# Performance work log

Hardware: AMD Instinct MI355X
Metric: run time of the kernel (lower is better)

Reference implementation:

```python
import jax, jax.numpy as jnp
import numpy as np
from jax import lax

TAU = 2.0
VTH = 1.0
EPS = 1e-5


def heaviside(x):
    return (x >= 0.0).astype(x.dtype)


def lif_scan(x):
    """x: [T, ...]; LIF with decay_input=True, v_reset=0 (hard reset)."""
    def step(v, xt):
        v = v + (xt - v) / TAU
        s = heaviside(v - VTH)
        v = v * (1.0 - s)
        return v, s
    _, out = lax.scan(step, jnp.zeros_like(x[0]), x)
    return out


def conv2d(x, w):
    return lax.conv_general_dilated(x, w, (1, 1), 'SAME',
                                    dimension_numbers=('NCHW', 'OIHW', 'NCHW'))


def bn(x, g, b, m, v):
    inv = lax.rsqrt(v + EPS)
    return (x - m[None, :, None, None]) * (g * inv)[None, :, None, None] + b[None, :, None, None]


def maxpool2(x):
    return lax.reduce_window(x, -jnp.inf, lax.max, (1, 1, 2, 2), (1, 1, 2, 2), 'VALID')


def conv_block(x, w, g, b, m, v, pool):
    T, B = x.shape[:2]
    y = x.reshape((T * B,) + x.shape[2:])
    y = bn(conv2d(y, w), g, b, m, v)
    y = y.reshape((T, B) + y.shape[1:])
    y = lif_scan(y)
    if pool:
        y = y.reshape((T * B,) + y.shape[2:])
        y = maxpool2(y)
        y = y.reshape((T, B) + y.shape[1:])
    return y


def setup_inputs() -> dict:
    key = jax.random.key(0)
    ks = jax.random.split(key, 12)
    x = jax.random.normal(ks[0], (8, 128, 3, 32, 32), jnp.float32)
    w1 = jax.random.normal(ks[1], (64, 3, 3, 3), jnp.float32) * 0.1
    w2 = jax.random.normal(ks[2], (128, 64, 3, 3), jnp.float32) * 0.05
    w3 = jax.random.normal(ks[3], (256, 128, 3, 3), jnp.float32) * 0.05
    fc1_w = jax.random.normal(ks[4], (512, 16384), jnp.float32) * 0.01
    raw = jax.random.normal(ks[5], (10, 512), jnp.float32)
    Q, _ = jnp.linalg.qr(raw.T)  # 10 <= 512: orthogonal prototypes
    protos = Q.T[:10]
    d = dict(x=x, w1=w1, w2=w2, w3=w3, fc1_w=fc1_w, protos=protos)
    for i, c in zip((1, 2, 3), (64, 128, 256)):
        d[f'g{i}'] = jnp.ones((c,), jnp.float32)
        d[f'b{i}'] = jnp.zeros((c,), jnp.float32)
        d[f'm{i}'] = jax.random.normal(jax.random.fold_in(key, 100 + i), (c,), jnp.float32) * 0.1
        d[f'var{i}'] = jax.random.uniform(jax.random.fold_in(key, 200 + i), (c,), jnp.float32) + 0.5
    return d


def reference(x, w1, g1, b1, m1, var1, w2, g2, b2, m2, var2,
              w3, g3, b3, m3, var3, fc1_w, protos):
    h = conv_block(x, w1, g1, b1, m1, var1, pool=False)   # [T,B,64,32,32]
    h = conv_block(h, w2, g2, b2, m2, var2, pool=True)    # [T,B,128,16,16]
    h = conv_block(h, w3, g3, b3, m3, var3, pool=True)    # [T,B,256,8,8]
    T, B = h.shape[:2]
    h = h.reshape(T, B, -1)                               # [T,B,16384]
    h = jnp.einsum('tbd,fd->tbf', h, fc1_w)
    h = lif_scan(h)                                        # [T,B,512]
    feat = h.mean(axis=0)                                  # [B,512]
    fn = feat / jnp.clip(jnp.linalg.norm(feat, axis=1, keepdims=True), 1e-12)
    pn = protos / jnp.clip(jnp.linalg.norm(protos, axis=1, keepdims=True), 1e-12)
    return fn @ pn.T * 10.0                                # [B,10]
```

## Files before the change

kernel.cpp:

```cpp
#include <hip/hip_runtime.h>
#include <stdint.h>

#define EPS 1e-5f

typedef __attribute__((ext_vector_type(4))) float f32x4;
typedef __attribute__((ext_vector_type(8))) __bf16 bf16x8;

__device__ __forceinline__ void gl_lds16(const void* g, void* l) {
    __builtin_amdgcn_global_load_lds(
        (const __attribute__((address_space(1))) void*)g,
        (__attribute__((address_space(3))) void*)l, 16, 0, 0);
}

__device__ __forceinline__ unsigned short f2bf(float f) {
    unsigned u = __builtin_bit_cast(unsigned, f);
    unsigned r = (u + 0x7FFFu + ((u >> 16) & 1u)) >> 16;
    return (unsigned short)r;
}
__device__ __forceinline__ float bf2f(unsigned short h) {
    unsigned u = ((unsigned)h) << 16;
    return __builtin_bit_cast(float, u);
}

__device__ __forceinline__ uint4 expand8(unsigned int bt) {
    uint4 val;
    val.x = ((bt & 1u) ? 0x3F80u : 0u)  | ((bt & 2u) ? 0x3F800000u : 0u);
    val.y = ((bt & 4u) ? 0x3F80u : 0u)  | ((bt & 8u) ? 0x3F800000u : 0u);
    val.z = ((bt & 16u) ? 0x3F80u : 0u) | ((bt & 32u) ? 0x3F800000u : 0u);
    val.w = ((bt & 64u) ? 0x3F80u : 0u) | ((bt & 128u) ? 0x3F800000u : 0u);
    return val;
}

#define OFF_W2S   0ULL
#define OFF_W3S   442368ULL
#define OFF_FCS   2211840ULL
#define OFF_S1M   52543488ULL
#define OFF_S2PM  60932096ULL
#define OFF_S3    65126400ULL
#define OFF_PRE4P 98680832ULL
#define OFF_FEAT  115458048ULL
#define OFF_PN    115720192ULL

__global__ void repack_w2s(const float* __restrict__ w2, unsigned short* __restrict__ out) {
    int i = blockIdx.x * 256 + threadIdx.x;
    if (i >= 73728) return;
    int oc = i / 576, rem = i % 576;
    int ic = rem / 9, tap = rem % 9;
    float w = w2[i];
    unsigned short hi = f2bf(w);  float r1 = w - bf2f(hi);
    unsigned short md = f2bf(r1); float r2 = r1 - bf2f(md);
    unsigned short lo = f2bf(r2);
    size_t base = ((size_t)(tap * 128 + oc)) * 64 + (((ic >> 3) ^ (oc & 7)) << 3) + (ic & 7);
    out[base] = hi; out[base + 73728] = md; out[base + 147456] = lo;
}
__global__ void repack_w3s(const float* __restrict__ w3, unsigned short* __restrict__ out) {
    int i = blockIdx.x * 256 + threadIdx.x;
    if (i >= 294912) return;
    int oc = i / 1152, rem = i % 1152;
    int ic = rem / 9, tap = rem % 9;
    float w = w3[i];
    unsigned short hi = f2bf(w);  float r1 = w - bf2f(hi);
    unsigned short md = f2bf(r1); float r2 = r1 - bf2f(md);
    unsigned short lo = f2bf(r2);
    int cc = tap * 2 + (ic >> 6), icl = ic & 63;
    size_t base = ((size_t)(cc * 256 + oc)) * 64 + (((icl >> 3) ^ (oc & 7)) << 3) + (icl & 7);
    out[base] = hi; out[base + 294912] = md; out[base + 589824] = lo;
}
__global__ void repack_fcs(const float* __restrict__ fw, unsigned short* __restrict__ out) {
    int i = blockIdx.x * 256 + threadIdx.x;
    if (i >= 8388608) return;
    int f = i >> 14, d = i & 16383;
    float w = fw[i];
    unsigned short hi = f2bf(w);  float r1 = w - bf2f(hi);
    unsigned short md = f2bf(r1); float r2 = r1 - bf2f(md);
    unsigned short lo = f2bf(r2);
    int cc = d >> 6, kl = d & 63;
    size_t base = (((size_t)cc << 9) + f) * 64 + (((kl >> 3) ^ (f & 7)) << 3) + (kl & 7);
    out[base] = hi; out[base + 8388608] = md; out[base + 16777216] = lo;
}

__global__ __launch_bounds__(256) void conv1_lif_pack(
    const float* __restrict__ x, const float* __restrict__ w1,
    const float* __restrict__ g1, const float* __restrict__ b1,
    const float* __restrict__ m1, const float* __restrict__ var1,
    unsigned long long* __restrict__ s1m)
{
    __shared__ float xt[3][3][40];
    int blk = blockIdx.x;
    int b = blk >> 5, y = blk & 31;
    int tid = threadIdx.x;
    int w = tid >> 6, lane = tid & 63;

    float wr[27];
#pragma unroll
    for (int j = 0; j < 27; ++j) wr[j] = w1[lane * 27 + j];
    float scale = g1[lane] / sqrtf(var1[lane] + EPS);
    float bias  = b1[lane] - m1[lane] * scale;

    float v[8];
#pragma unroll
    for (int p = 0; p < 8; ++p) v[p] = 0.f;

    for (int t = 0; t < 8; ++t) {
        __syncthreads();
        const float* xb = x + ((size_t)(t * 128 + b)) * 3072;
        for (int i = tid; i < 360; i += 256) {
            int ic = i / 120, rem = i % 120, dr = rem / 40, col = rem % 40;
            int yy = y + dr - 1, xx = col - 4;
            float val = 0.f;
            if (yy >= 0 && yy < 32 && xx >= 0 && xx < 32)
                val = xb[ic * 1024 + yy * 32 + xx];
            xt[ic][dr][col] = val;
        }
        __syncthreads();

        float acc[8];
#pragma unroll
        for (int p = 0; p < 8; ++p) acc[p] = 0.f;
#pragma unroll
        for (int ic = 0; ic < 3; ++ic)
#pragma unroll
        for (int dr = 0; dr < 3; ++dr) {
            const float* row = &xt[ic][dr][w * 8];
            float bf[16];
            *(float4*)&bf[0]  = *(const float4*)&row[0];
            *(float4*)&bf[4]  = *(const float4*)&row[4];
            *(float4*)&bf[8]  = *(const float4*)&row[8];
            *(float4*)&bf[12] = *(const float4*)&row[12];
#pragma unroll
            for (int p = 0; p < 8; ++p)
#pragma unroll
                for (int dxm = 0; dxm < 3; ++dxm)
                    acc[p] += bf[p + dxm + 3] * wr[ic * 9 + dr * 3 + dxm];
        }
        size_t base = ((size_t)t * 128 + b) * 1024 + y * 32 + w * 8;
#pragma unroll
        for (int p = 0; p < 8; ++p) {
            float pre = acc[p] * scale + bias;
            v[p] = v[p] + (pre - v[p]) * 0.5f;
            bool s = (v[p] >= 1.0f);
            unsigned long long mk = __ballot(s);
            if (s) v[p] = 0.f;
            if (lane == 0) s1m[base + p] = mk;
        }
    }
}

__global__ __launch_bounds__(512, 2) void conv2_mfma(
    const unsigned long long* __restrict__ s1m,
    const unsigned short* __restrict__ w2s,
    const float* __restrict__ g, const float* __restrict__ bb,
    const float* __restrict__ mm, const float* __restrict__ vv,
    unsigned long long* __restrict__ s2pm)
{
    __shared__ unsigned long long mt[2][340];
    __shared__ unsigned short Aexp[340 * 64];
    __shared__ unsigned short Bt[2][3 * 8192];
    __shared__ unsigned short pm16[4][16][8];

    int tid = threadIdx.x;
    int m0 = blockIdx.x << 8;
    int b = m0 >> 10;
    int pix0 = m0 & 1023;
    int y0 = pix0 >> 5;

    int w = tid >> 6, lane = tid & 63;
    int wm = w & 3, wn = w >> 2;
    int q = lane >> 4, r = lane & 15;
    int swr = r & 7;

    int yloc[4], xloc[4];
#pragma unroll
    for (int i = 0; i < 4; ++i) {
        int mrow = wm * 64 + i * 16 + r;
        yloc[i] = mrow >> 5; xloc[i] = mrow & 31;
    }

    float scl[4], bia[4];
#pragma unroll
    for (int j = 0; j < 4; ++j) {
        int oc = wn * 64 + j * 16 + r;
        float s0 = g[oc] / sqrtf(vv[oc] + EPS);
        scl[j] = s0;
        bia[j] = bb[oc] - mm[oc] * s0;
    }

    float vr[4][4][4];
#pragma unroll
    for (int i = 0; i < 4; ++i)
#pragma unroll
        for (int j = 0; j < 4; ++j)
#pragma unroll
            for (int k = 0; k < 4; ++k) vr[i][j][k] = 0.f;

    const char* w2sb = (const char*)w2s;
    char* Btb = (char*)Bt;

    for (int i = tid; i < 340; i += 512) {
        int ly = i / 34, lx = i % 34;
        int yy = y0 + ly - 1, xx = lx - 1;
        unsigned long long mv = 0ULL;
        if (yy >= 0 && yy < 32 && xx >= 0 && xx < 32)
            mv = s1m[(b << 10) + (yy << 5) + xx];
        mt[0][i] = mv;
    }
#pragma unroll
    for (int s = 0; s < 3; ++s)
#pragma unroll
        for (int p = 0; p < 2; ++p)
            gl_lds16(w2sb + s * 147456 + p * 8192 + (w << 10) + (lane << 4),
                     Btb + s * 16384 + p * 8192 + (w << 10));
    __syncthreads();

    int pp = 0;
    for (int t = 0; t < 8; ++t) {
        {
            const unsigned long long* mtc = mt[t & 1];
            for (int u = tid; u < 680; u += 512) {
                int p = u >> 1, hc = u & 1;
                unsigned long long mk = mtc[p];
                unsigned int w32 = (unsigned int)(mk >> (hc << 5));
#pragma unroll
                for (int c4 = 0; c4 < 4; ++c4) {
                    int c = (hc << 2) + c4;
                    *(uint4*)((char*)Aexp + p * 128 + ((c ^ (p & 7)) << 4)) =
                        expand8(w32 >> (c4 << 3));
                }
            }
        }
        if (t < 7) {
            for (int i = tid; i < 340; i += 512) {
                int ly = i / 34, lx = i % 34;
                int yy = y0 + ly - 1, xx = lx - 1;
                unsigned long long mv = 0ULL;
                if (yy >= 0 && yy < 32 && xx >= 0 && xx < 32)
                    mv = s1m[(size_t)(t + 1) * 131072 + (b << 10) + (yy << 5) + xx];
                mt[(t + 1) & 1][i] = mv;
            }
        }
        __syncthreads();

        f32x4 acc[4][4];
#pragma unroll
        for (int i = 0; i < 4; ++i)
#pragma unroll
            for (int j = 0; j < 4; ++j) acc[i][j] = (f32x4){0.f, 0.f, 0.f, 0.f};

        for (int tap = 0; tap < 9; ++tap) {
            int dy = tap / 3, dx = tap - dy * 3;
            {
                int tap2 = (tap == 8) ? 0 : (tap + 1);
                const char* gb = w2sb + tap2 * 16384 + (w << 10) + (lane << 4);
                char* lb = Btb + (pp ^ 1) * 49152 + (w << 10);
#pragma unroll
                for (int s = 0; s < 3; ++s)
#pragma unroll
                    for (int p = 0; p < 2; ++p)
                        gl_lds16(gb + s * 147456 + p * 8192, lb + s * 16384 + p * 8192);
            }
            const char* Bc = Btb + pp * 49152;
#pragma unroll
            for (int ks = 0; ks < 2; ++ks) {
                bf16x8 af[4];
#pragma unroll
                for (int i = 0; i < 4; ++i) {
                    int p3 = (yloc[i] + dy) * 34 + xloc[i] + dx;
                    af[i] = *(const bf16x8*)((const char*)Aexp + p3 * 128 +
                             ((((ks << 2) + q) ^ (p3 & 7)) << 4));
                }
#pragma unroll
                for (int s = 0; s < 3; ++s) {
                    bf16x8 bfr[4];
#pragma unroll
                    for (int j = 0; j < 4; ++j)
                        bfr[j] = *(const bf16x8*)(Bc + s * 16384 + (wn * 64 + j * 16 + r) * 128 +
                                 ((((ks << 2) + q) ^ swr) << 4));
#pragma unroll
                    for (int i = 0; i < 4; ++i)
#pragma unroll
                        for (int j = 0; j < 4; ++j)
                            acc[i][j] = __builtin_amdgcn_mfma_f32_16x16x32_bf16(af[i], bfr[j], acc[i][j], 0, 0, 0);
                }
            }
            __syncthreads();
            pp ^= 1;
        }

        unsigned long long S = 0ULL;
#pragma unroll
        for (int i = 0; i < 4; ++i)
#pragma unroll
            for (int j = 0; j < 4; ++j)
#pragma unroll
                for (int reg = 0; reg < 4; ++reg) {
                    float pre = acc[i][j][reg] * scl[j] + bia[j];
                    float vo = vr[i][j][reg];
                    vo = vo + (pre - vo) * 0.5f;
                    bool sp = (vo >= 1.0f);
                    vr[i][j][reg] = sp ? 0.f : vo;
                    if (sp) S |= 1ULL << (i * 16 + j * 4 + reg);
                }
#pragma unroll
        for (int b1 = 0; b1 < 2; ++b1)
#pragma unroll
            for (int u = 0; u < 2; ++u)
#pragma unroll
                for (int j = 0; j < 4; ++j) {
                    int k0 = b1 * 16 + j * 4 + 2 * u;
                    bool sp = (((S >> k0) | (S >> (k0 + 1)) | (S >> (k0 + 32)) | (S >> (k0 + 33))) & 1ULL) != 0;
                    unsigned long long mk = __ballot(sp);
                    if (r == 0)
                        pm16[wm][b1 * 8 + (q << 1) + u][wn * 4 + j] = (unsigned short)(mk >> (q << 4));
                }
        __syncthreads();
        if (tid < 128) {
            int py = tid >> 5, px = (tid >> 1) & 15, h = tid & 1;
            unsigned long long vmk = *(unsigned long long*)&pm16[py][px][h << 2];
            s2pm[(size_t)t * 65536 + ((size_t)(b << 8) + ((y0 >> 1) + py) * 16 + px) * 2 + h] = vmk;
        }
    }
}

__global__ __launch_bounds__(512, 2) void conv3_mfma(
    const unsigned long long* __restrict__ s2pm,
    const unsigned short* __restrict__ w3s,
    const float* __restrict__ g, const float* __restrict__ bb,
    const float* __restrict__ mm, const float* __restrict__ vv,
    unsigned short* __restrict__ s3)
{
    __shared__ unsigned long long mt3[2][324][2];
    __shared__ unsigned short Aexp[324 * 64];
    __shared__ unsigned short Bt[2][3 * 8192];

    int tid = threadIdx.x;
    int b = blockIdx.x;
    int n0 = blockIdx.y << 7;

    int w = tid >> 6, lane = tid & 63;
    int wm = w & 3, wn = w >> 2;
    int q = lane >> 4, r = lane & 15;
    int swr = r & 7;

    float scl[4], bia[4];
#pragma unroll
    for (int j = 0; j < 4; ++j) {
        int oc = n0 + wn * 64 + j * 16 + r;
        float s0 = g[oc] / sqrtf(vv[oc] + EPS);
        scl[j] = s0;
        bia[j] = bb[oc] - mm[oc] * s0;
    }

    float vr[4][4][4];
#pragma unroll
    for (int i = 0; i < 4; ++i)
#pragma unroll
        for (int j = 0; j < 4; ++j)
#pragma unroll
            for (int k = 0; k < 4; ++k) vr[i][j][k] = 0.f;

    const char* w3sb = (const char*)w3s;
    char* Btb = (char*)Bt;
    int bsw = b & 7;

    for (int i = tid; i < 648; i += 512) {
        int p = i >> 1, hh = i & 1;
        int ly = p / 18, lx = p % 18;
        int yy = ly - 1, xx = lx - 1;
        unsigned long long mv = 0ULL;
        if (yy >= 0 && yy < 16 && xx >= 0 && xx < 16)
            mv = s2pm[((size_t)(b << 8) + (yy << 4) + xx) * 2 + hh];
        mt3[0][p][hh] = mv;
    }
#pragma unroll
    for (int s = 0; s < 3; ++s)
#pragma unroll
        for (int p = 0; p < 2; ++p)
            gl_lds16(w3sb + s * 589824 + n0 * 128 + p * 8192 + (w << 10) + (lane << 4),
                     Btb + s * 16384 + p * 8192 + (w << 10));
    __syncthreads();

    int pp = 0;
    for (int t = 0; t < 8; ++t) {
        {
            for (int u = tid; u < 648; u += 512) {
                int p = u >> 1, hc = u & 1;
                unsigned long long mk = mt3[t & 1][p][0];
                unsigned int w32 = (unsigned int)(mk >> (hc << 5));
#pragma unroll
                for (int c4 = 0; c4 < 4; ++c4) {
                    int c = (hc << 2) + c4;
                    *(uint4*)((char*)Aexp + p * 128 + ((c ^ (p & 7)) << 4)) =
                        expand8(w32 >> (c4 << 3));
                }
            }
        }
        if (t < 7) {
            for (int i = tid; i < 648; i += 512) {
                int p = i >> 1, hh = i & 1;
                int ly = p / 18, lx = p % 18;
                int yy = ly - 1, xx = lx - 1;
                unsigned long long mv = 0ULL;
                if (yy >= 0 && yy < 16 && xx >= 0 && xx < 16)
                    mv = s2pm[(size_t)(t + 1) * 65536 + ((size_t)(b << 8) + (yy << 4) + xx) * 2 + hh];
                mt3[(t + 1) & 1][p][hh] = mv;
            }
        }
        __syncthreads();

        f32x4 acc[4][4];
#pragma unroll
        for (int i = 0; i < 4; ++i)
#pragma unroll
            for (int j = 0; j < 4; ++j) acc[i][j] = (f32x4){0.f, 0.f, 0.f, 0.f};

        for (int h = 0; h < 2; ++h) {
            for (int tap = 0; tap < 9; ++tap) {
                int dy = tap / 3, dx = tap - dy * 3;
                int cc = tap * 2 + h;
                {
                    int ncc = (tap < 8) ? (cc + 2) : ((h == 0) ? 1 : 0);
                    const char* gb = w3sb + ncc * 32768 + n0 * 128 + (w << 10) + (lane << 4);
                    char* lb = Btb + (pp ^ 1) * 49152 + (w << 10);
#pragma unroll
                    for (int s = 0; s < 3; ++s)
#pragma unroll
                        for (int p = 0; p < 2; ++p)
                            gl_lds16(gb + s * 589824 + p * 8192, lb + s * 16384 + p * 8192);
                }
                const char* Bc = Btb + pp * 49152;
#pragma unroll
                for (int ks = 0; ks < 2; ++ks) {
                    bf16x8 af[4];
#pragma unroll
                    for (int i = 0; i < 4; ++i) {
                        int p3 = (wm * 4 + i + dy) * 18 + r + dx;
                        af[i] = *(const bf16x8*)((const char*)Aexp + p3 * 128 +
                                 ((((ks << 2) + q) ^ (p3 & 7)) << 4));
                    }
#pragma unroll
                    for (int s = 0; s < 3; ++s) {
                        bf16x8 bfr[4];
#pragma unroll
                        for (int j = 0; j < 4; ++j)
                            bfr[j] = *(const bf16x8*)(Bc + s * 16384 + (wn * 64 + j * 16 + r) * 128 +
                                     ((((ks << 2) + q) ^ swr) << 4));
#pragma unroll
                        for (int i = 0; i < 4; ++i)
#pragma unroll
                            for (int j = 0; j < 4; ++j)
                                acc[i][j] = __builtin_amdgcn_mfma_f32_16x16x32_bf16(af[i], bfr[j], acc[i][j], 0, 0, 0);
                    }
                }
                __syncthreads();
                pp ^= 1;
            }
            if (h == 0) {
                for (int u = tid; u < 648; u += 512) {
                    int p = u >> 1, hc = u & 1;
                    unsigned long long mk = mt3[t & 1][p][1];
                    unsigned int w32 = (unsigned int)(mk >> (hc << 5));
#pragma unroll
                    for (int c4 = 0; c4 < 4; ++c4) {
                        int c = (hc << 2) + c4;
                        *(uint4*)((char*)Aexp + p * 128 + ((c ^ (p & 7)) << 4)) =
                            expand8(w32 >> (c4 << 3));
                    }
                }
                __syncthreads();
            }
        }

        unsigned long long S = 0ULL;
#pragma unroll
        for (int i = 0; i < 4; ++i)
#pragma unroll
            for (int j = 0; j < 4; ++j)
#pragma unroll
                for (int reg = 0; reg < 4; ++reg) {
                    float pre = acc[i][j][reg] * scl[j] + bia[j];
                    float vo = vr[i][j][reg];
                    vo = vo + (pre - vo) * 0.5f;
                    bool sp = (vo >= 1.0f);
                    vr[i][j][reg] = sp ? 0.f : vo;
                    if (sp) S |= 1ULL << (i * 16 + j * 4 + reg);
                }
        unsigned short* s3t = s3 + (size_t)t * 2097152;
#pragma unroll
        for (int a2 = 0; a2 < 2; ++a2)
#pragma unroll
            for (int u = 0; u < 2; ++u)
#pragma unroll
                for (int j = 0; j < 4; ++j) {
                    int kA = 32 * a2 + j * 4 + 2 * u;
                    bool sp = (((S >> kA) | (S >> (kA + 1)) | (S >> (kA + 16)) | (S >> (kA + 17))) & 1ULL) != 0;
                    int oc = n0 + wn * 64 + j * 16 + r;
                    int y2 = wm * 2 + a2;
                    int x2 = (q << 1) + u;
                    s3t[(size_t)(b << 14) + oc * 64 + ((y2 ^ bsw) << 3) + x2] =
                        (unsigned short)(sp ? 0x3F80 : 0);
                }
    }
}

__global__ __launch_bounds__(256, 2) void fc_mfma(
    const unsigned short* __restrict__ s3,
    const unsigned short* __restrict__ fcs,
    float* __restrict__ pre4p)
{
    __shared__ unsigned short A[128 * 64];
    __shared__ unsigned short B[3 * 128 * 64];

    int tid = threadIdx.x;
    int m0 = blockIdx.x << 7;
    int n0 = blockIdx.y << 7;
    int kseg = blockIdx.z;
    int cc0 = kseg << 5;

    int w = tid >> 6, lane = tid & 63;
    int wm = w & 1, wn = w >> 1;
    int q = lane >> 4, r = lane & 15;
    int swr = r & 7;

    f32x4 acc[4][4];
#pragma unroll
    for (int i = 0; i < 4; ++i)
#pragma unroll
        for (int j = 0; j < 4; ++j) acc[i][j] = (f32x4){0.f, 0.f, 0.f, 0.f};

    const char* s3b = (const char*)s3;
    const char* fcsb = (const char*)fcs;

    for (int cc = cc0; cc < cc0 + 32; ++cc) {
        __syncthreads();
        {
            char* lb = (char*)A + (w << 12);
#pragma unroll
            for (int p = 0; p < 4; ++p)
                gl_lds16(s3b + (size_t)(m0 + w * 32 + p * 8 + (lane >> 3)) * 32768
                             + cc * 128 + ((lane & 7) << 4),
                         lb + (p << 10));
        }
        {
            const char* gb = fcsb + cc * 65536 + n0 * 128 + (w << 12) + (lane << 4);
            char* lb = (char*)B + (w << 12);
#pragma unroll
            for (int s = 0; s < 3; ++s)
#pragma unroll
                for (int p = 0; p < 4; ++p)
                    gl_lds16(gb + s * 16777216 + (p << 10), lb + s * 16384 + (p << 10));
        }
        __syncthreads();
#pragma unroll
        for (int ks = 0; ks < 2; ++ks) {
            bf16x8 af[4];
#pragma unroll
            for (int i = 0; i < 4; ++i)
                af[i] = *(const bf16x8*)((const char*)A + (wm * 64 + i * 16 + r) * 128 + ((((ks << 2) + q) ^ swr) << 4));
#pragma unroll
            for (int s = 0; s < 3; ++s) {
                bf16x8 bfr[4];
#pragma unroll
                for (int j = 0; j < 4; ++j)
                    bfr[j] = *(const bf16x8*)((const char*)B + s * 16384 + (wn * 64 + j * 16 + r) * 128 + ((((ks << 2) + q) ^ swr) << 4));
#pragma unroll
                for (int i = 0; i < 4; ++i)
#pragma unroll
                    for (int j = 0; j < 4; ++j)
                        acc[i][j] = __builtin_amdgcn_mfma_f32_16x16x32_bf16(af[i], bfr[j], acc[i][j], 0, 0, 0);
            }
        }
    }
#pragma unroll
    for (int i = 0; i < 4; ++i) {
#pragma unroll
        for (int j = 0; j < 4; ++j) {
            size_t base = ((size_t)kseg * 1024 + m0 + wm * 64 + i * 16 + (q << 2)) * 512
                        + n0 + wn * 64 + j * 16 + r;
#pragma unroll
            for (int reg = 0; reg < 4; ++reg)
                pre4p[base + (size_t)reg * 512] = acc[i][j][reg];
        }
    }
}

__global__ void lif4_mean(const float* __restrict__ P, float* __restrict__ feat) {
    int i = blockIdx.x * 256 + threadIdx.x;
    if (i >= 65536) return;
    int b = i >> 9, f = i & 511;
    float v = 0.f, sum = 0.f;
#pragma unroll
    for (int t = 0; t < 8; ++t) {
        float pre = 0.f;
#pragma unroll
        for (int s = 0; s < 8; ++s)
            pre += P[(size_t)s * 524288 + (size_t)(t * 128 + b) * 512 + f];
        v = v + (pre - v) * 0.5f;
        if (v >= 1.0f) { sum += 1.f; v = 0.f; }
    }
    feat[i] = sum * 0.125f;
}

__global__ void protos_norm(const float* __restrict__ P, float* __restrict__ pn) {
    int p = blockIdx.x;
    int lane = threadIdx.x;
    float ss = 0.f;
    for (int f = lane; f < 512; f += 64) { float x = P[p * 512 + f]; ss += x * x; }
#pragma unroll
    for (int o = 32; o > 0; o >>= 1) ss += __shfl_xor(ss, o);
    float inv = 1.f / fmaxf(sqrtf(ss), 1e-12f);
    for (int f = lane; f < 512; f += 64) pn[p * 512 + f] = P[p * 512 + f] * inv;
}

__global__ void final_logits(const float* __restrict__ feat, const float* __restrict__ pn,
                             float* __restrict__ out) {
    int b = blockIdx.x;
    int lane = threadIdx.x;
    float fr[8];
    float ss = 0.f;
#pragma unroll
    for (int j = 0; j < 8; ++j) { fr[j] = feat[b * 512 + j * 64 + lane]; ss += fr[j] * fr[j]; }
#pragma unroll
    for (int o = 32; o > 0; o >>= 1) ss += __shfl_xor(ss, o);
    float inv = 10.f / fmaxf(sqrtf(ss), 1e-12f);
    for (int p = 0; p < 10; ++p) {
        float d = 0.f;
#pragma unroll
        for (int j = 0; j < 8; ++j) d += fr[j] * pn[p * 512 + j * 64 + lane];
#pragma unroll
        for (int o = 32; o > 0; o >>= 1) d += __shfl_xor(d, o);
        if (lane == 0) out[b * 10 + p] = d * inv;
    }
}

extern "C" void kernel_launch(void* const* d_in, const int* in_sizes, int n_in,
                              void* d_out, int out_size, void* d_ws, size_t ws_size,
                              hipStream_t stream) {
    const float* x      = (const float*)d_in[0];
    const float* w1     = (const float*)d_in[1];
    const float* w2     = (const float*)d_in[2];
    const float* w3     = (const float*)d_in[3];
    const float* fc1    = (const float*)d_in[4];
    const float* protos = (const float*)d_in[5];
    const float* g1 = (const float*)d_in[6],  *b1 = (const float*)d_in[7];
    const float* m1 = (const float*)d_in[8],  *v1 = (const float*)d_in[9];
    const float* g2 = (const float*)d_in[10], *b2 = (const float*)d_in[11];
    const float* m2 = (const float*)d_in[12], *v2p = (const float*)d_in[13];
    const float* g3 = (const float*)d_in[14], *b3 = (const float*)d_in[15];
    const float* m3 = (const float*)d_in[16], *v3p = (const float*)d_in[17];

    char* ws = (char*)d_ws;
    unsigned short* w2s = (unsigned short*)(ws + OFF_W2S);
    unsigned short* w3s = (unsigned short*)(ws + OFF_W3S);
    unsigned short* fcs = (unsigned short*)(ws + OFF_FCS);
    unsigned long long* s1m  = (unsigned long long*)(ws + OFF_S1M);
    unsigned long long* s2pm = (unsigned long long*)(ws + OFF_S2PM);
    unsigned short* s3 = (unsigned short*)(ws + OFF_S3);
    float* pre4p = (float*)(ws + OFF_PRE4P);
    float* feat  = (float*)(ws + OFF_FEAT);
    float* pn    = (float*)(ws + OFF_PN);

    repack_w2s<<<288, 256, 0, stream>>>(w2, w2s);
    repack_w3s<<<1152, 256, 0, stream>>>(w3, w3s);
    repack_fcs<<<32768, 256, 0, stream>>>(fc1, fcs);

    conv1_lif_pack<<<4096, 256, 0, stream>>>(x, w1, g1, b1, m1, v1, s1m);
    conv2_mfma<<<512, 512, 0, stream>>>(s1m, w2s, g2, b2, m2, v2p, s2pm);
    conv3_mfma<<<dim3(128, 2), 512, 0, stream>>>(s2pm, w3s, g3, b3, m3, v3p, s3);

    fc_mfma<<<dim3(8, 4, 8), 256, 0, stream>>>(s3, fcs, pre4p);
    lif4_mean<<<256, 256, 0, stream>>>(pre4p, feat);
    protos_norm<<<10, 64, 0, stream>>>(protos, pn);
    final_logits<<<128, 64, 0, stream>>>(feat, pn, (float*)d_out);
}
```

Baseline: 938.2 us.

## Halve conv tiles, read conv weights directly from global, double fc split-K

Conv2 and conv3 now use 256-thread blocks covering half as many output pixels, so twice as many blocks launch. The LDS double-buffered weight staging and its per-tap barriers are removed; weights are unswizzled and each wave loads its B fragments straight from global memory. The fc split-K factor doubles to 16 segments, with the partial-sum buffer and the reduction grown to match. This trades LDS traffic and synchronisation for more parallelism, at the cost of more global or L2 weight reads and extra partial-sum traffic.

```diff
diff --git a/kernel.cpp b/kernel.cpp
--- a/kernel.cpp
+++ b/kernel.cpp
@@ -38,8 +38,8 @@
 #define OFF_S2PM  60932096ULL
 #define OFF_S3    65126400ULL
 #define OFF_PRE4P 98680832ULL
-#define OFF_FEAT  115458048ULL
-#define OFF_PN    115720192ULL
+#define OFF_FEAT  132235264ULL
+#define OFF_PN    132497408ULL
 
 __global__ void repack_w2s(const float* __restrict__ w2, unsigned short* __restrict__ out) {
     int i = blockIdx.x * 256 + threadIdx.x;
@@ -50,7 +50,7 @@
     unsigned short hi = f2bf(w);  float r1 = w - bf2f(hi);
     unsigned short md = f2bf(r1); float r2 = r1 - bf2f(md);
     unsigned short lo = f2bf(r2);
-    size_t base = ((size_t)(tap * 128 + oc)) * 64 + (((ic >> 3) ^ (oc & 7)) << 3) + (ic & 7);
+    size_t base = ((size_t)(tap * 128 + oc)) * 64 + ic;
     out[base] = hi; out[base + 73728] = md; out[base + 147456] = lo;
 }
 __global__ void repack_w3s(const float* __restrict__ w3, unsigned short* __restrict__ out) {
@@ -63,7 +63,7 @@
     unsigned short md = f2bf(r1); float r2 = r1 - bf2f(md);
     unsigned short lo = f2bf(r2);
     int cc = tap * 2 + (ic >> 6), icl = ic & 63;
-    size_t base = ((size_t)(cc * 256 + oc)) * 64 + (((icl >> 3) ^ (oc & 7)) << 3) + (icl & 7);
+    size_t base = ((size_t)(cc * 256 + oc)) * 64 + icl;
     out[base] = hi; out[base + 294912] = md; out[base + 589824] = lo;
 }
 __global__ void repack_fcs(const float* __restrict__ fw, unsigned short* __restrict__ out) {
@@ -146,28 +146,26 @@
     }
 }
 
-__global__ __launch_bounds__(512, 2) void conv2_mfma(
+__global__ __launch_bounds__(256, 2) void conv2_mfma(
     const unsigned long long* __restrict__ s1m,
     const unsigned short* __restrict__ w2s,
     const float* __restrict__ g, const float* __restrict__ bb,
     const float* __restrict__ mm, const float* __restrict__ vv,
     unsigned long long* __restrict__ s2pm)
 {
-    __shared__ unsigned long long mt[2][340];
-    __shared__ unsigned short Aexp[340 * 64];
-    __shared__ unsigned short Bt[2][3 * 8192];
-    __shared__ unsigned short pm16[4][16][8];
+    __shared__ unsigned long long mt[2][204];
+    __shared__ unsigned short Aexp[204 * 64];
+    __shared__ unsigned short pm16[2][16][8];
 
     int tid = threadIdx.x;
-    int m0 = blockIdx.x << 8;
+    int m0 = blockIdx.x << 7;
     int b = m0 >> 10;
     int pix0 = m0 & 1023;
     int y0 = pix0 >> 5;
 
     int w = tid >> 6, lane = tid & 63;
-    int wm = w & 3, wn = w >> 2;
+    int wm = w & 1, wn = w >> 1;
     int q = lane >> 4, r = lane & 15;
-    int swr = r & 7;
 
     int yloc[4], xloc[4];
 #pragma unroll
@@ -194,9 +192,8 @@
             for (int k = 0; k < 4; ++k) vr[i][j][k] = 0.f;
 
     const char* w2sb = (const char*)w2s;
-    char* Btb = (char*)Bt;
-
-    for (int i = tid; i < 340; i += 512) {
+
+    for (int i = tid; i < 204; i += 256) {
         int ly = i / 34, lx = i % 34;
         int yy = y0 + ly - 1, xx = lx - 1;
         unsigned long long mv = 0ULL;
@@ -204,19 +201,12 @@
             mv = s1m[(b << 10) + (yy << 5) + xx];
         mt[0][i] = mv;
     }
-#pragma unroll
-    for (int s = 0; s < 3; ++s)
-#pragma unroll
-        for (int p = 0; p < 2; ++p)
-            gl_lds16(w2sb + s * 147456 + p * 8192 + (w << 10) + (lane << 4),
-                     Btb + s * 16384 + p * 8192 + (w << 10));
     __syncthreads();
 
-    int pp = 0;
     for (int t = 0; t < 8; ++t) {
         {
             const unsigned long long* mtc = mt[t & 1];
-            for (int u = tid; u < 680; u += 512) {
+            for (int u = tid; u < 408; u += 256) {
                 int p = u >> 1, hc = u & 1;
                 unsigned long long mk = mtc[p];
                 unsigned int w32 = (unsigned int)(mk >> (hc << 5));
@@ -229,7 +219,7 @@
             }
         }
         if (t < 7) {
-            for (int i = tid; i < 340; i += 512) {
+            for (int i = tid; i < 204; i += 256) {
                 int ly = i / 34, lx = i % 34;
                 int yy = y0 + ly - 1, xx = lx - 1;
                 unsigned long long mv = 0ULL;
@@ -246,19 +236,10 @@
 #pragma unroll
             for (int j = 0; j < 4; ++j) acc[i][j] = (f32x4){0.f, 0.f, 0.f, 0.f};
 
+#pragma unroll 1
         for (int tap = 0; tap < 9; ++tap) {
             int dy = tap / 3, dx = tap - dy * 3;
-            {
-                int tap2 = (tap == 8) ? 0 : (tap + 1);
-                const char* gb = w2sb + tap2 * 16384 + (w << 10) + (lane << 4);
-                char* lb = Btb + (pp ^ 1) * 49152 + (w << 10);
-#pragma unroll
-                for (int s = 0; s < 3; ++s)
-#pragma unroll
-                    for (int p = 0; p < 2; ++p)
-                        gl_lds16(gb + s * 147456 + p * 8192, lb + s * 16384 + p * 8192);
-            }
-            const char* Bc = Btb + pp * 49152;
+            const char* wt = w2sb + tap * 16384 + (wn * 64 + r) * 128 + q * 16;
 #pragma unroll
             for (int ks = 0; ks < 2; ++ks) {
                 bf16x8 af[4];
@@ -273,8 +254,7 @@
                     bf16x8 bfr[4];
 #pragma unroll
                     for (int j = 0; j < 4; ++j)
-                        bfr[j] = *(const bf16x8*)(Bc + s * 16384 + (wn * 64 + j * 16 + r) * 128 +
-                                 ((((ks << 2) + q) ^ swr) << 4));
+                        bfr[j] = *(const bf16x8*)(wt + s * 147456 + (j << 11) + (ks << 6));
 #pragma unroll
                     for (int i = 0; i < 4; ++i)
 #pragma unroll
@@ -282,8 +262,6 @@
                             acc[i][j] = __builtin_amdgcn_mfma_f32_16x16x32_bf16(af[i], bfr[j], acc[i][j], 0, 0, 0);
                 }
             }
-            __syncthreads();
-            pp ^= 1;
         }
 
         unsigned long long S = 0ULL;
@@ -313,7 +291,7 @@
                         pm16[wm][b1 * 8 + (q << 1) + u][wn * 4 + j] = (unsigned short)(mk >> (q << 4));
                 }
         __syncthreads();
-        if (tid < 128) {
+        if (tid < 64) {
             int py = tid >> 5, px = (tid >> 1) & 15, h = tid & 1;
             unsigned long long vmk = *(unsigned long long*)&pm16[py][px][h << 2];
             s2pm[(size_t)t * 65536 + ((size_t)(b << 8) + ((y0 >> 1) + py) * 16 + px) * 2 + h] = vmk;
@@ -321,25 +299,33 @@
     }
 }
 
-__global__ __launch_bounds__(512, 2) void conv3_mfma(
+__global__ __launch_bounds__(256, 2) void conv3_mfma(
     const unsigned long long* __restrict__ s2pm,
     const unsigned short* __restrict__ w3s,
     const float* __restrict__ g, const float* __restrict__ bb,
     const float* __restrict__ mm, const float* __restrict__ vv,
     unsigned short* __restrict__ s3)
 {
-    __shared__ unsigned long long mt3[2][324][2];
-    __shared__ unsigned short Aexp[324 * 64];
-    __shared__ unsigned short Bt[2][3 * 8192];
+    __shared__ unsigned long long mt3[2][180][2];
+    __shared__ unsigned short Aexp[180 * 64];
 
     int tid = threadIdx.x;
-    int b = blockIdx.x;
+    int m0 = blockIdx.x << 7;
     int n0 = blockIdx.y << 7;
+    int b = m0 >> 8;
+    int pix0 = m0 & 255;
+    int y0 = pix0 >> 4;
 
     int w = tid >> 6, lane = tid & 63;
-    int wm = w & 3, wn = w >> 2;
+    int wm = w & 1, wn = w >> 1;
     int q = lane >> 4, r = lane & 15;
-    int swr = r & 7;
+
+    int yloc[4], xloc[4];
+#pragma unroll
+    for (int i = 0; i < 4; ++i) {
+        int mrow = wm * 64 + i * 16 + r;
+        yloc[i] = mrow >> 4; xloc[i] = mrow & 15;
+    }
 
     float scl[4], bia[4];
 #pragma unroll
@@ -359,46 +345,36 @@
             for (int k = 0; k < 4; ++k) vr[i][j][k] = 0.f;
 
     const char* w3sb = (const char*)w3s;
-    char* Btb = (char*)Bt;
     int bsw = b & 7;
 
-    for (int i = tid; i < 648; i += 512) {
+    for (int i = tid; i < 360; i += 256) {
         int p = i >> 1, hh = i & 1;
         int ly = p / 18, lx = p % 18;
-        int yy = ly - 1, xx = lx - 1;
+        int yy = y0 + ly - 1, xx = lx - 1;
         unsigned long long mv = 0ULL;
         if (yy >= 0 && yy < 16 && xx >= 0 && xx < 16)
             mv = s2pm[((size_t)(b << 8) + (yy << 4) + xx) * 2 + hh];
         mt3[0][p][hh] = mv;
     }
-#pragma unroll
-    for (int s = 0; s < 3; ++s)
-#pragma unroll
-        for (int p = 0; p < 2; ++p)
-            gl_lds16(w3sb + s * 589824 + n0 * 128 + p * 8192 + (w << 10) + (lane << 4),
-                     Btb + s * 16384 + p * 8192 + (w << 10));
-    __syncthreads();
-
-    int pp = 0;
+
     for (int t = 0; t < 8; ++t) {
-        {
-            for (int u = tid; u < 648; u += 512) {
-                int p = u >> 1, hc = u & 1;
-                unsigned long long mk = mt3[t & 1][p][0];
-                unsigned int w32 = (unsigned int)(mk >> (hc << 5));
-#pragma unroll
-                for (int c4 = 0; c4 < 4; ++c4) {
-                    int c = (hc << 2) + c4;
-                    *(uint4*)((char*)Aexp + p * 128 + ((c ^ (p & 7)) << 4)) =
-                        expand8(w32 >> (c4 << 3));
-                }
+        __syncthreads();
+        for (int u = tid; u < 360; u += 256) {
+            int p = u >> 1, hc = u & 1;
+            unsigned long long mk = mt3[t & 1][p][0];
+            unsigned int w32 = (unsigned int)(mk >> (hc << 5));
+#pragma unroll
+            for (int c4 = 0; c4 < 4; ++c4) {
+                int c = (hc << 2) + c4;
+                *(uint4*)((char*)Aexp + p * 128 + ((c ^ (p & 7)) << 4)) =
+                    expand8(w32 >> (c4 << 3));
             }
         }
         if (t < 7) {
-            for (int i = tid; i < 648; i += 512) {
+            for (int i = tid; i < 360; i += 256) {
                 int p = i >> 1, hh = i & 1;
                 int ly = p / 18, lx = p % 18;
-                int yy = ly - 1, xx = lx - 1;
+                int yy = y0 + ly - 1, xx = lx - 1;
                 unsigned long long mv = 0ULL;
                 if (yy >= 0 && yy < 16 && xx >= 0 && xx < 16)
                     mv = s2pm[(size_t)(t + 1) * 65536 + ((size_t)(b << 8) + (yy << 4) + xx) * 2 + hh];
@@ -414,26 +390,17 @@
             for (int j = 0; j < 4; ++j) acc[i][j] = (f32x4){0.f, 0.f, 0.f, 0.f};
 
         for (int h = 0; h < 2; ++h) {
+#pragma unroll 1
             for (int tap = 0; tap < 9; ++tap) {
                 int dy = tap / 3, dx = tap - dy * 3;
                 int cc = tap * 2 + h;
-                {
-                    int ncc = (tap < 8) ? (cc + 2) : ((h == 0) ? 1 : 0);
-                    const char* gb = w3sb + ncc * 32768 + n0 * 128 + (w << 10) + (lane << 4);
-                    char* lb = Btb + (pp ^ 1) * 49152 + (w << 10);
-#pragma unroll
-                    for (int s = 0; s < 3; ++s)
-#pragma unroll
-                        for (int p = 0; p < 2; ++p)
-                            gl_lds16(gb + s * 589824 + p * 8192, lb + s * 16384 + p * 8192);
-                }
-                const char* Bc = Btb + pp * 49152;
+                const char* wt = w3sb + cc * 32768 + (n0 + wn * 64 + r) * 128 + q * 16;
 #pragma unroll
                 for (int ks = 0; ks < 2; ++ks) {
                     bf16x8 af[4];
 #pragma unroll
                     for (int i = 0; i < 4; ++i) {
-                        int p3 = (wm * 4 + i + dy) * 18 + r + dx;
+                        int p3 = (yloc[i] + dy) * 18 + xloc[i] + dx;
                         af[i] = *(const bf16x8*)((const char*)Aexp + p3 * 128 +
                                  ((((ks << 2) + q) ^ (p3 & 7)) << 4));
                     }
@@ -442,8 +409,7 @@
                         bf16x8 bfr[4];
 #pragma unroll
                         for (int j = 0; j < 4; ++j)
-                            bfr[j] = *(const bf16x8*)(Bc + s * 16384 + (wn * 64 + j * 16 + r) * 128 +
-                                     ((((ks << 2) + q) ^ swr) << 4));
+                            bfr[j] = *(const bf16x8*)(wt + s * 589824 + (j << 11) + (ks << 6));
 #pragma unroll
                         for (int i = 0; i < 4; ++i)
 #pragma unroll
@@ -451,11 +417,10 @@
                                 acc[i][j] = __builtin_amdgcn_mfma_f32_16x16x32_bf16(af[i], bfr[j], acc[i][j], 0, 0, 0);
                     }
                 }
+            }
+            if (h == 0) {
                 __syncthreads();
-                pp ^= 1;
-            }
-            if (h == 0) {
-                for (int u = tid; u < 648; u += 512) {
+                for (int u = tid; u < 360; u += 256) {
                     int p = u >> 1, hc = u & 1;
                     unsigned long long mk = mt3[t & 1][p][1];
                     unsigned int w32 = (unsigned int)(mk >> (hc << 5));
@@ -494,7 +459,7 @@
                     int kA = 32 * a2 + j * 4 + 2 * u;
                     bool sp = (((S >> kA) | (S >> (kA + 1)) | (S >> (kA + 16)) | (S >> (kA + 17))) & 1ULL) != 0;
                     int oc = n0 + wn * 64 + j * 16 + r;
-                    int y2 = wm * 2 + a2;
+                    int y2 = (y0 >> 1) + wm * 2 + a2;
                     int x2 = (q << 1) + u;
                     s3t[(size_t)(b << 14) + oc * 64 + ((y2 ^ bsw) << 3) + x2] =
                         (unsigned short)(sp ? 0x3F80 : 0);
@@ -514,7 +479,7 @@
     int m0 = blockIdx.x << 7;
     int n0 = blockIdx.y << 7;
     int kseg = blockIdx.z;
-    int cc0 = kseg << 5;
+    int cc0 = kseg << 4;
 
     int w = tid >> 6, lane = tid & 63;
     int wm = w & 1, wn = w >> 1;
@@ -530,7 +495,7 @@
     const char* s3b = (const char*)s3;
     const char* fcsb = (const char*)fcs;
 
-    for (int cc = cc0; cc < cc0 + 32; ++cc) {
+    for (int cc = cc0; cc < cc0 + 16; ++cc) {
         __syncthreads();
         {
             char* lb = (char*)A + (w << 12);
@@ -592,7 +557,7 @@
     for (int t = 0; t < 8; ++t) {
         float pre = 0.f;
 #pragma unroll
-        for (int s = 0; s < 8; ++s)
+        for (int s = 0; s < 16; ++s)
             pre += P[(size_t)s * 524288 + (size_t)(t * 128 + b) * 512 + f];
         v = v + (pre - v) * 0.5f;
         if (v >= 1.0f) { sum += 1.f; v = 0.f; }
@@ -664,10 +629,10 @@
     repack_fcs<<<32768, 256, 0, stream>>>(fc1, fcs);
 
     conv1_lif_pack<<<4096, 256, 0, stream>>>(x, w1, g1, b1, m1, v1, s1m);
-    conv2_mfma<<<512, 512, 0, stream>>>(s1m, w2s, g2, b2, m2, v2p, s2pm);
-    conv3_mfma<<<dim3(128, 2), 512, 0, stream>>>(s2pm, w3s, g3, b3, m3, v3p, s3);
-
-    fc_mfma<<<dim3(8, 4, 8), 256, 0, stream>>>(s3, fcs, pre4p);
+    conv2_mfma<<<1024, 256, 0, stream>>>(s1m, w2s, g2, b2, m2, v2p, s2pm);
+    conv3_mfma<<<dim3(256, 2), 256, 0, stream>>>(s2pm, w3s, g3, b3, m3, v3p, s3);
+
+    fc_mfma<<<dim3(8, 4, 16), 256, 0, stream>>>(s3, fcs, pre4p);
     lif4_mean<<<256, 256, 0, stream>>>(pre4p, feat);
     protos_norm<<<10, 64, 0, stream>>>(protos, pn);
     final_logits<<<128, 64, 0, stream>>>(feat, pn, (float*)d_out);
```

New measurement: 1.924 ms. 2.05x slower.
